# Kernel optimization log

Hardware: AMD Instinct MI355X
Metric: run time of the kernel (lower is better)

## Reference

```python
import jax, jax.numpy as jnp
import numpy as np

B, S, E, H = 4, 2048, 1024, 16
D = E // H

def setup_inputs() -> dict:
    key = jax.random.key(0)
    ks = jax.random.split(key, 8)
    sc = lambda fan_in: 1.0 / np.sqrt(fan_in)
    return {
        "query": jax.random.normal(ks[0], (B, S, E), jnp.float32),
        "Wq": jax.random.normal(ks[1], (E, E), jnp.float32) * sc(E),
        "bq": jnp.zeros((E,), jnp.float32),
        "Wk": jax.random.normal(ks[2], (E, E), jnp.float32) * sc(E),
        "bk": jnp.zeros((E,), jnp.float32),
        "Wv": jax.random.normal(ks[3], (E, E), jnp.float32) * sc(E),
        "bv": jnp.zeros((E,), jnp.float32),
        "Wo": jax.random.normal(ks[4], (E, E), jnp.float32) * sc(E),
        "bo": jnp.zeros((E,), jnp.float32),
        "Wm1": jax.random.normal(ks[5], (E // 4, E), jnp.float32) * sc(E),
        "bm1": jnp.zeros((E // 4,), jnp.float32),
        "Wm2": jax.random.normal(ks[6], (E, E // 4), jnp.float32) * sc(E // 4),
        "bm2": jnp.zeros((E,), jnp.float32),
        "dopamine": jnp.ones((1,), jnp.float32),
        "serotonin": jnp.ones((1,), jnp.float32),
        "norepinephrine": jnp.ones((1,), jnp.float32),
        "acetylcholine": jnp.ones((1,), jnp.float32),
        "attn_scale": jnp.ones((1,), jnp.float32),
        "attn_bias": jnp.zeros((1,), jnp.float32),
    }

def reference(query, Wq, bq, Wk, bk, Wv, bv, Wo, bo,
              Wm1, bm1, Wm2, bm2,
              dopamine, serotonin, norepinephrine, acetylcholine,
              attn_scale, attn_bias):
    scale = D ** (-0.5)
    # projections (nn.Linear: y = x @ W.T + b)
    q = (query @ Wq.T + bq).reshape(B, S, H, D).transpose(0, 2, 1, 3)  # [B,H,S,D]
    k = (query @ Wk.T + bk).reshape(B, S, H, D).transpose(0, 2, 1, 3)
    v = (query @ Wv.T + bv).reshape(B, S, H, D).transpose(0, 2, 1, 3)
    scores = jnp.einsum('bhqd,bhkd->bhqk', q, k) * scale  # [B,H,S,S]
    probs = jax.nn.softmax(scores, axis=-1)
    attn = jnp.einsum('bhqk,bhkd->bhqd', probs, v)  # [B,H,S,D]
    # neuromodulation: MLP on query, summed scalar-weighted effects / 4
    mod = jax.nn.relu(query @ Wm1.T + bm1) @ Wm2.T + bm2  # [B,S,E]
    nm_gain = (dopamine + serotonin + norepinephrine + acetylcholine) / 4.0  # [1]
    neuromod = (mod * nm_gain).reshape(B, S, H, D).transpose(0, 2, 1, 3)  # [B,H,S,D]
    attn = (attn * attn_scale + attn_bias) * (1.0 + neuromod)
    attn = attn.transpose(0, 2, 1, 3).reshape(B, S, E)
    return attn @ Wo.T + bo
```

## Files before the change

### kernel.cpp

```cpp
#include <hip/hip_runtime.h>
#include <hip/hip_bf16.h>
#include <cstdint>

#define PB 4
#define PS 2048
#define PE 1024
#define PH 16
#define PD 64
#define PM (PB * PS)

typedef __attribute__((ext_vector_type(8))) _Float16 half8;
typedef __attribute__((ext_vector_type(4))) float f32x4;

#define MFMAH __builtin_amdgcn_mfma_f32_16x16x32_f16

#define GLOAD_LDS(gp, lp) __builtin_amdgcn_global_load_lds(                    \
    (const __attribute__((address_space(1))) void*)(gp),                       \
    (__attribute__((address_space(3))) void*)(lp), 16, 0, 0)

#if __has_builtin(__builtin_amdgcn_exp2f)
#define FAST_EXP2 1
#define QSC (0.125f * 1.4426950408889634f)
#define FTHR 11.5415603f
#define EXP_P(x) __builtin_amdgcn_exp2f(x)
#else
#define FAST_EXP2 0
#define QSC 0.125f
#define FTHR 8.f
#define EXP_P(x) __expf(x)
#endif

__device__ inline unsigned short h16(float x) {
    _Float16 h = (_Float16)x;
    unsigned short u;
    __builtin_memcpy(&u, &h, 2);
    return u;
}
__device__ inline float f16tof(unsigned short u) {
    _Float16 h;
    __builtin_memcpy(&h, &u, 2);
    return (float)h;
}
__device__ inline unsigned pkrtz(float a, float b) {
    auto p = __builtin_amdgcn_cvt_pkrtz(a, b);
    unsigned u;
    __builtin_memcpy(&u, &p, 4);
    return u;
}

__global__ __launch_bounds__(256)
void split_all(const float* __restrict__ q,   const float* __restrict__ wq,
               const float* __restrict__ wk,  const float* __restrict__ wv,
               const float* __restrict__ wo,  const float* __restrict__ wm1,
               const float* __restrict__ wm2,
               unsigned short* qh,  unsigned short* wqh, unsigned short* wkh,
               unsigned short* wvh, unsigned short* woh,
               unsigned short* m1h, unsigned short* m2h)
{
    const int b = blockIdx.x;
    const float* src; unsigned short* dst; int base;
    if      (b <  8192) { src = q;   dst = qh;  base = 0;     }
    else if (b <  9216) { src = wq;  dst = wqh; base = 8192;  }
    else if (b < 10240) { src = wk;  dst = wkh; base = 9216;  }
    else if (b < 11264) { src = wv;  dst = wvh; base = 10240; }
    else if (b < 12288) { src = wo;  dst = woh; base = 11264; }
    else if (b < 12544) { src = wm1; dst = m1h; base = 12288; }
    else                { src = wm2; dst = m2h; base = 12544; }
    const int i = (b - base) * 256 + threadIdx.x;
    float4 f = ((const float4*)src)[i];
    ushort4 h;
    h.x = h16(f.x); h.y = h16(f.y); h.z = h16(f.z); h.w = h16(f.w);
    ((ushort4*)dst)[i] = h;
}

__global__ __launch_bounds__(512, 2)
void gemm_qkv(const unsigned short* __restrict__ Ah,
              const unsigned short* __restrict__ Wqh,
              const unsigned short* __restrict__ Wkh,
              const unsigned short* __restrict__ Wvh,
              const float* __restrict__ bq, const float* __restrict__ bk,
              const float* __restrict__ bv,
              unsigned short* __restrict__ qh16, unsigned short* __restrict__ kf,
              unsigned short* __restrict__ vtf)
{
    __shared__ int4 ldsq[8192];
    char* const lds = (char*)ldsq;
    const int K = PE;

    const int tid  = threadIdx.x;
    const int lane = tid & 63;
    const int w    = tid >> 6;
    const int lq   = lane & 15;
    const int lg   = lane >> 4;
    const int wr   = w >> 2;
    const int wc   = w & 3;
    const int m0   = blockIdx.x * 128;
    const int n0   = blockIdx.y * 128;

    const int plane = w >> 1;
    const unsigned short* const gp =
        (plane == 0) ? Ah  + (size_t)m0 * K :
        (plane == 1) ? Wqh + (size_t)n0 * K :
        (plane == 2) ? Wkh + (size_t)n0 * K :
                       Wvh + (size_t)n0 * K;
    const int pbase = plane * 16384;
    const int ch0   = (w & 1) * 8;
    const int scol8 = (((lane & 7) ^ (lane >> 3)) << 3);
    const int lrow8 = lane >> 3;

    auto ISSUE = [&](int k0, int bufn) {
        #pragma unroll
        for (int r = 0; r < 8; ++r) {
            const int c   = ch0 + r;
            const int row = c * 8 + lrow8;
            GLOAD_LDS(gp + (size_t)row * K + k0 + scol8,
                      lds + bufn * 65536 + pbase + c * 1024 + 16 * lane);
        }
    };

    f32x4 acc[3][4][2];
    #pragma unroll
    for (int o = 0; o < 3; ++o)
        #pragma unroll
        for (int mt = 0; mt < 4; ++mt)
            #pragma unroll
            for (int nt = 0; nt < 2; ++nt)
                acc[o][mt][nt] = (f32x4){0.f, 0.f, 0.f, 0.f};

    ISSUE(0, 0);
    __syncthreads();

    int buf = 0;
    for (int k0 = 0; k0 < K; k0 += 64) {
        if (k0 + 64 < K) ISSUE(k0 + 64, buf ^ 1);

        const char* const L = lds + buf * 65536;
        #pragma unroll
        for (int kh = 0; kh < 2; ++kh) {
            half8 af[4];
            #pragma unroll
            for (int mt = 0; mt < 4; ++mt) {
                const int row = 64 * wr + 16 * mt + lq;
                const int off = row * 128 + ((kh * 64 + 16 * lg) ^ ((row & 7) << 4));
                af[mt] = *(const half8*)(L + off);
            }
            #pragma unroll
            for (int o = 0; o < 3; ++o) {
                #pragma unroll
                for (int nt = 0; nt < 2; ++nt) {
                    const int row = 32 * wc + 16 * nt + lq;
                    const int off = row * 128 + ((kh * 64 + 16 * lg) ^ ((row & 7) << 4));
                    half8 bf = *(const half8*)(L + 16384 * (o + 1) + off);
                    #pragma unroll
                    for (int mt = 0; mt < 4; ++mt)
                        acc[o][mt][nt] = MFMAH(af[mt], bf, acc[o][mt][nt], 0, 0, 0);
                }
            }
        }
        __syncthreads();
        buf ^= 1;
    }

    #pragma unroll
    for (int nt = 0; nt < 2; ++nt) {
        const int n = n0 + 32 * wc + 16 * nt + lq;
        const int h = n >> 6, d = n & 63;
        const float bqv = bq[n], bkv = bk[n], bvv = bv[n];
        #pragma unroll
        for (int mt = 0; mt < 4; ++mt) {
            #pragma unroll
            for (int j = 0; j < 4; ++j) {
                const int m = m0 + 64 * wr + 16 * mt + 4 * lg + j;
                const int b = m >> 11, s = m & 2047;
                qh16[((size_t)(b * PH + h) * PS + s) * PD + d] =
                    h16((acc[0][mt][nt][j] + bqv) * QSC);
                kf[((size_t)(b * PH + h) * PS + s) * PD + d] =
                    h16(acc[1][mt][nt][j] + bkv);
                const int scol = (s & ~63) + ((mt & 1) << 5) + (lg << 3)
                               + ((mt >> 1) << 2) + j;
                vtf[((size_t)(b * PH + h) * PD + d) * PS + scol] =
                    h16(acc[2][mt][nt][j] + bvv);
            }
        }
    }
}

template<int MODE, bool RELU>
__global__ __launch_bounds__(256, 2)
void gemm_pl(const unsigned short* __restrict__ Ah,
             const unsigned short* __restrict__ Bh,
             const float* __restrict__ bias, float* __restrict__ C,
             unsigned short* __restrict__ Oh,
             int M, int N, int K)
{
    __shared__ int4 ldsq[4096];
    char* const lds = (char*)ldsq;

    const int tid  = threadIdx.x;
    const int lane = tid & 63;
    const int w    = tid >> 6;
    const int lq   = lane & 15;
    const int lg   = lane >> 4;
    const int wm   = (w >> 1) * 64;
    const int wn   = (w & 1) * 64;
    const int m0   = blockIdx.x * 128;
    const int n0   = blockIdx.y * 128;

    const unsigned short* const gp =
        (w < 2) ? Ah + (size_t)m0 * K : Bh + (size_t)n0 * K;
    const int pb    = (w < 2) ? 0 : 16384;
    const int ch0   = (w & 1) * 8;
    const int scol8 = (((lane & 7) ^ (lane >> 3)) << 3);
    const int lrow8 = lane >> 3;

    auto ISSUE = [&](int k0, int bufn) {
        #pragma unroll
        for (int r = 0; r < 8; ++r) {
            const int c   = ch0 + r;
            const int row = c * 8 + lrow8;
            GLOAD_LDS(gp + (size_t)row * K + k0 + scol8,
                      lds + bufn * 32768 + pb + c * 1024 + 16 * lane);
        }
    };

    f32x4 acc[4][4];
    #pragma unroll
    for (int mt = 0; mt < 4; ++mt)
        #pragma unroll
        for (int nt = 0; nt < 4; ++nt)
            acc[mt][nt] = (f32x4){0.f, 0.f, 0.f, 0.f};

    ISSUE(0, 0);
    __syncthreads();

    int buf = 0;
    for (int k0 = 0; k0 < K; k0 += 64) {
        if (k0 + 64 < K) ISSUE(k0 + 64, buf ^ 1);

        const char* const L = lds + buf * 32768;
        #pragma unroll
        for (int kh = 0; kh < 2; ++kh) {
            half8 af[4];
            #pragma unroll
            for (int mt = 0; mt < 4; ++mt) {
                const int row = wm + 16 * mt + lq;
                const int off = row * 128 + ((kh * 64 + 16 * lg) ^ ((row & 7) << 4));
                af[mt] = *(const half8*)(L + off);
            }
            #pragma unroll
            for (int nt = 0; nt < 4; ++nt) {
                const int row = wn + 16 * nt + lq;
                const int off = row * 128 + ((kh * 64 + 16 * lg) ^ ((row & 7) << 4));
                half8 bf = *(const half8*)(L + 16384 + off);
                #pragma unroll
                for (int mt = 0; mt < 4; ++mt)
                    acc[mt][nt] = MFMAH(af[mt], bf, acc[mt][nt], 0, 0, 0);
            }
        }
        __syncthreads();
        buf ^= 1;
    }

    #pragma unroll
    for (int nt = 0; nt < 4; ++nt) {
        const int n  = n0 + wn + 16 * nt + lq;
        const float bv = bias[n];
        #pragma unroll
        for (int mt = 0; mt < 4; ++mt) {
            #pragma unroll
            for (int j = 0; j < 4; ++j) {
                const int m = m0 + wm + 16 * mt + 4 * lg + j;
                float v = acc[mt][nt][j] + bv;
                if (RELU) v = fmaxf(v, 0.f);
                if (MODE == 0) {
                    C[(size_t)m * N + n] = v;
                } else {
                    Oh[(size_t)m * N + n] = h16(v);
                }
            }
        }
    }
}

typedef __attribute__((ext_vector_type(8))) short short8;
#define MFMA16 __builtin_amdgcn_mfma_f32_16x16x32_bf16
__device__ inline unsigned short bf16rn(float x) {
    unsigned u = __builtin_bit_cast(unsigned, x);
    u += 0x7FFFu + ((u >> 16) & 1u);
    return (unsigned short)(u >> 16);
}
__device__ inline float bf16tof(unsigned short h) {
    unsigned u = ((unsigned)h) << 16;
    return __builtin_bit_cast(float, u);
}
__device__ inline void split2(float x, unsigned short& h, unsigned short& l) {
    h = bf16rn(x);
    l = bf16rn(x - bf16tof(h));
}

template<int MODE, bool RELU>
__global__ __launch_bounds__(256, 2)
void gemm_nt(const float* __restrict__ A, const float* __restrict__ Bw,
             const float* __restrict__ bias, float* __restrict__ C,
             unsigned short* __restrict__ Ohi,
             int M, int N, int K,
             const float* __restrict__ attn,
             const float* __restrict__ g0, const float* __restrict__ g1,
             const float* __restrict__ g2, const float* __restrict__ g3,
             const float* __restrict__ asc, const float* __restrict__ abi)
{
    __shared__ int4 ldsq[4096];
    char* const lds = (char*)ldsq;

    const int tid  = threadIdx.x;
    const int lane = tid & 63;
    const int w    = tid >> 6;
    const int lq   = lane & 15;
    const int lg   = lane >> 4;
    const int wm   = (w >> 1) * 64;
    const int wn   = (w & 1) * 64;
    const int m0   = blockIdx.x * 128;
    const int n0   = blockIdx.y * 128;

    const int irow = tid >> 3;
    const int ic8  = (tid & 7) * 8;
    const int woff = (ic8 * 2);

    f32x4 acc[4][4];
    #pragma unroll
    for (int mt = 0; mt < 4; ++mt)
        #pragma unroll
        for (int nt = 0; nt < 4; ++nt)
            acc[mt][nt] = (f32x4){0.f, 0.f, 0.f, 0.f};

    for (int k0 = 0; k0 < K; k0 += 64) {
        #pragma unroll
        for (int mat = 0; mat < 2; ++mat) {
            const float* const src = mat ? Bw : A;
            const int rbase = mat ? n0 : m0;
            const int pbase = mat ? 32768 : 0;
            #pragma unroll
            for (int r = 0; r < 4; ++r) {
                const int row = irow + 32 * r;
                const float* p = src + (size_t)(rbase + row) * K + k0 + ic8;
                float4 f0 = *(const float4*)p;
                float4 f1 = *(const float4*)(p + 4);
                short8 vh, vl;
                {
                    unsigned short h, l;
                    split2(f0.x, h, l); vh[0] = (short)h; vl[0] = (short)l;
                    split2(f0.y, h, l); vh[1] = (short)h; vl[1] = (short)l;
                    split2(f0.z, h, l); vh[2] = (short)h; vl[2] = (short)l;
                    split2(f0.w, h, l); vh[3] = (short)h; vl[3] = (short)l;
                    split2(f1.x, h, l); vh[4] = (short)h; vl[4] = (short)l;
                    split2(f1.y, h, l); vh[5] = (short)h; vl[5] = (short)l;
                    split2(f1.z, h, l); vh[6] = (short)h; vl[6] = (short)l;
                    split2(f1.w, h, l); vh[7] = (short)h; vl[7] = (short)l;
                }
                const int off = row * 128 + (woff ^ ((row & 7) << 4));
                *(short8*)(lds + pbase + off)         = vh;
                *(short8*)(lds + pbase + 16384 + off) = vl;
            }
        }
        __syncthreads();

        #pragma unroll
        for (int kh = 0; kh < 2; ++kh) {
            short8 afh[4], afl[4];
            #pragma unroll
            for (int mt = 0; mt < 4; ++mt) {
                const int row = wm + 16 * mt + lq;
                const int off = row * 128 + ((kh * 64 + 16 * lg) ^ ((row & 7) << 4));
                afh[mt] = *(const short8*)(lds + off);
                afl[mt] = *(const short8*)(lds + 16384 + off);
            }
            #pragma unroll
            for (int nt = 0; nt < 4; ++nt) {
                const int row = wn + 16 * nt + lq;
                const int off = row * 128 + ((kh * 64 + 16 * lg) ^ ((row & 7) << 4));
                short8 bfh = *(const short8*)(lds + 32768 + off);
                short8 bfl = *(const short8*)(lds + 49152 + off);
                #pragma unroll
                for (int mt = 0; mt < 4; ++mt) {
                    acc[mt][nt] = MFMA16(afh[mt], bfh, acc[mt][nt], 0, 0, 0);
                    acc[mt][nt] = MFMA16(afh[mt], bfl, acc[mt][nt], 0, 0, 0);
                    acc[mt][nt] = MFMA16(afl[mt], bfh, acc[mt][nt], 0, 0, 0);
                }
            }
        }
        __syncthreads();
    }

    float gain = 0.f, ascv = 0.f, abiv = 0.f;
    if (MODE == 2) {
        gain = 0.25f * (*g0 + *g1 + *g2 + *g3);
        ascv = *asc;
        abiv = *abi;
    }

    #pragma unroll
    for (int nt = 0; nt < 4; ++nt) {
        const int n  = n0 + wn + 16 * nt + lq;
        const float bv = bias[n];
        #pragma unroll
        for (int mt = 0; mt < 4; ++mt) {
            #pragma unroll
            for (int j = 0; j < 4; ++j) {
                const int m = m0 + wm + 16 * mt + 4 * lg + j;
                float v = acc[mt][nt][j] + bv;
                if (RELU) v = fmaxf(v, 0.f);
                if (MODE == 0) {
                    C[(size_t)m * N + n] = v;
                } else if (MODE == 1) {
                    const int b = m >> 11, s = m & 2047;
                    const int h = n >> 6, d = n & 63;
                    Ohi[((size_t)(b * PH + h) * PS + s) * PD + d] = h16(v * QSC);
                } else if (MODE == 3) {
                    const int b = m >> 11, s = m & 2047;
                    const int h = n >> 6, d = n & 63;
                    Ohi[((size_t)(b * PH + h) * PS + s) * PD + d] = h16(v);
                } else if (MODE == 4) {
                    const int b = m >> 11;
                    const int h = n >> 6, d = n & 63;
                    const int scol = (m & 2047 & ~63) + ((mt & 1) << 5)
                                   + (lg << 3) + ((mt >> 1) << 2) + j;
                    Ohi[((size_t)(b * PH + h) * PD + d) * PS + scol] = h16(v);
                } else {
                    const int b = m >> 11, s = m & 2047;
                    const int h = n >> 6, d = n & 63;
                    const float av = attn[((size_t)(b * PH + h) * PS + s) * PD + d];
                    C[(size_t)m * N + n] = (av * ascv + abiv) * (1.f + v * gain);
                }
            }
        }
    }
}

template<int FUSE>
__global__ __launch_bounds__(256, 4)
void flash_mfma(const unsigned short* __restrict__ qh16,
                const unsigned short* __restrict__ kf,
                const unsigned short* __restrict__ vtf,
                const unsigned short* __restrict__ modh,
                const float* __restrict__ g0, const float* __restrict__ g1,
                const float* __restrict__ g2, const float* __restrict__ g3,
                const float* __restrict__ asc, const float* __restrict__ abi,
                unsigned short* __restrict__ afh, float* __restrict__ attn)
{
    __shared__ int4 ldsv[2048];
    char* const ldsb = (char*)ldsv;

    const int tid  = threadIdx.x;
    const int lane = tid & 63;
    const int w    = tid >> 6;
    const int lq   = lane & 15;
    const int lg   = lane >> 4;

    const int L  = blockIdx.x + (blockIdx.y << 4) + (blockIdx.z << 8);
    const int nL = ((L & 7) << 7) + (L >> 3);
    const int bh = nL >> 4;
    const int q0 = (nL & 15) * 128 + w * 32;

    const size_t kbase = (size_t)bh * PS * PD;
    const size_t vbase = (size_t)bh * PD * PS;

    const unsigned short* const gp = (w < 2) ? kf + kbase : vtf + vbase;
    const bool isK = (w < 2);
    const int ch0   = (w & 1) * 4;
    const int scol8 = (((lane & 7) ^ (lane >> 3)) << 3);
    const int lrow8 = lane >> 3;

    auto ISSUE = [&](int kt, int bufn) {
        #pragma unroll
        for (int r = 0; r < 4; ++r) {
            const int c   = ch0 + r;
            const int row = c * 8 + lrow8;
            const size_t goff = isK ? (size_t)(kt + row) * PD + scol8
                                    : (size_t)row * PS + kt + scol8;
            GLOAD_LDS(gp + goff,
                      ldsb + bufn * 16384 + (isK ? 0 : 8192) + c * 1024 + 16 * lane);
        }
    };

    const half8 onesh = {(_Float16)1.f, (_Float16)1.f, (_Float16)1.f,
                         (_Float16)1.f, (_Float16)1.f, (_Float16)1.f,
                         (_Float16)1.f, (_Float16)1.f};

    half8 qh[2][2];
    #pragma unroll
    for (int u = 0; u < 2; ++u) {
        const unsigned short* qp =
            qh16 + ((size_t)bh * PS + q0 + 16 * u + lq) * PD + 8 * lg;
        qh[u][0] = *(const half8*)(qp);
        qh[u][1] = *(const half8*)(qp + 32);
    }

    f32x4 ot[2][4];
    #pragma unroll
    for (int u = 0; u < 2; ++u)
        #pragma unroll
        for (int mt = 0; mt < 4; ++mt)
            ot[u][mt] = (f32x4){0.f, 0.f, 0.f, 0.f};
    f32x4 lacc[2] = {{0.f,0.f,0.f,0.f}, {0.f,0.f,0.f,0.f}};
    float m_run[2] = {0.f, 0.f};

    ISSUE(0, 0);
    __syncthreads();

    int buf = 0;
    for (int kti = 0; kti < PS / 64; ++kti) {
        const bool pf = (kti + 1 < PS / 64);
        if (pf) ISSUE((kti + 1) * 64, buf ^ 1);

        const char* const L2 = ldsb + buf * 16384;

        f32x4 st[2][4];
        __builtin_amdgcn_s_setprio(1);
        #pragma unroll
        for (int mt = 0; mt < 4; ++mt) {
            const int row = 16 * mt + lq;
            const int swz = (row & 7) << 4;
            const char* kr = L2 + row * 128;
            half8 a0 = *(const half8*)(kr + ((16 * lg) ^ swz));
            half8 a1 = *(const half8*)(kr + ((64 + 16 * lg) ^ swz));
            #pragma unroll
            for (int u = 0; u < 2; ++u) {
                const float nm = -m_run[u];
                f32x4 acc = {nm, nm, nm, nm};
                acc = MFMAH(a0, qh[u][0], acc, 0, 0, 0);
                acc = MFMAH(a1, qh[u][1], acc, 0, 0, 0);
                st[u][mt] = acc;
            }
        }
        __builtin_amdgcn_s_setprio(0);

        half8 pb[2][2];
        #pragma unroll
        for (int u = 0; u < 2; ++u) {
            float a0 = fmaxf(fmaxf(st[u][0][0], st[u][0][1]), st[u][0][2]);
            float a1 = fmaxf(fmaxf(st[u][0][3], st[u][1][0]), st[u][1][1]);
            float a2 = fmaxf(fmaxf(st[u][1][2], st[u][1][3]), st[u][2][0]);
            float a3 = fmaxf(fmaxf(st[u][2][1], st[u][2][2]), st[u][2][3]);
            float a4 = fmaxf(fmaxf(st[u][3][0], st[u][3][1]), st[u][3][2]);
            float b0 = fmaxf(fmaxf(a0, a1), a2);
            float b1 = fmaxf(fmaxf(a3, a4), st[u][3][3]);
            float lmax = fmaxf(b0, b1);
            if (!__all(lmax <= FTHR)) {
                float pmax = fmaxf(lmax, __shfl_xor(lmax, 16));
                pmax = fmaxf(pmax, __shfl_xor(pmax, 32));
                float corr = EXP_P(-pmax);
                m_run[u] += pmax;
                #pragma unroll
                for (int j = 0; j < 4; ++j)
                    lacc[u][j] *= corr;
                #pragma unroll
                for (int mt = 0; mt < 4; ++mt)
                    #pragma unroll
                    for (int j = 0; j < 4; ++j) {
                        ot[u][mt][j] *= corr;
                        st[u][mt][j] -= pmax;
                    }
            }
            #pragma unroll
            for (int mt = 0; mt < 4; ++mt)
                #pragma unroll
                for (int j = 0; j < 4; ++j)
                    st[u][mt][j] = EXP_P(st[u][mt][j]);
            #pragma unroll
            for (int t = 0; t < 2; ++t) {
                unsigned w0 = pkrtz(st[u][t][0],     st[u][t][1]);
                unsigned w1 = pkrtz(st[u][t][2],     st[u][t][3]);
                unsigned w2 = pkrtz(st[u][t + 2][0], st[u][t + 2][1]);
                unsigned w3 = pkrtz(st[u][t + 2][2], st[u][t + 2][3]);
                uint4 pw = make_uint4(w0, w1, w2, w3);
                __builtin_memcpy(&pb[u][t], &pw, 16);
            }
            lacc[u] = MFMAH(onesh, pb[u][0], lacc[u], 0, 0, 0);
            lacc[u] = MFMAH(onesh, pb[u][1], lacc[u], 0, 0, 0);
        }

        __builtin_amdgcn_s_setprio(1);
        #pragma unroll
        for (int t = 0; t < 2; ++t) {
            #pragma unroll
            for (int mt = 0; mt < 4; ++mt) {
                const int row = 16 * mt + lq;
                const int swz = (row & 7) << 4;
                const char* vr = L2 + 8192 + row * 128;
                half8 vv = *(const half8*)(vr + ((t * 64 + 16 * lg) ^ swz));
                #pragma unroll
                for (int u = 0; u < 2; ++u)
                    ot[u][mt] = MFMAH(vv, pb[u][t], ot[u][mt], 0, 0, 0);
            }
        }
        __builtin_amdgcn_s_setprio(0);

        __syncthreads();
        buf ^= 1;
    }

    if (FUSE) {
        const float gain = 0.25f * (*g0 + *g1 + *g2 + *g3);
        const float ascv = *asc, abiv = *abi;
        const int bb = bh >> 4, hh = bh & 15;
        #pragma unroll
        for (int u = 0; u < 2; ++u) {
            const int m = bb * PS + q0 + 16 * u + lq;
            const unsigned short* mp = modh + (size_t)m * PE + hh * 64 + 4 * lg;
            unsigned short* op = afh + (size_t)m * PE + hh * 64 + 4 * lg;
            const float inv = 1.f / lacc[u][0];
            #pragma unroll
            for (int mt = 0; mt < 4; ++mt) {
                ushort4 mv = *(const ushort4*)(mp + 16 * mt);
                ushort4 ov;
                ov.x = h16((ot[u][mt][0] * inv * ascv + abiv) * (1.f + f16tof(mv.x) * gain));
                ov.y = h16((ot[u][mt][1] * inv * ascv + abiv) * (1.f + f16tof(mv.y) * gain));
                ov.z = h16((ot[u][mt][2] * inv * ascv + abiv) * (1.f + f16tof(mv.z) * gain));
                ov.w = h16((ot[u][mt][3] * inv * ascv + abiv) * (1.f + f16tof(mv.w) * gain));
                *(ushort4*)(op + 16 * mt) = ov;
            }
        }
    } else {
        #pragma unroll
        for (int u = 0; u < 2; ++u) {
            const float inv = 1.f / lacc[u][0];
            float* op = attn + ((size_t)bh * PS + q0 + 16 * u + lq) * PD + 4 * lg;
            #pragma unroll
            for (int mt = 0; mt < 4; ++mt) {
                float4 o;
                o.x = ot[u][mt][0] * inv; o.y = ot[u][mt][1] * inv;
                o.z = ot[u][mt][2] * inv; o.w = ot[u][mt][3] * inv;
                *(float4*)(op + 16 * mt) = o;
            }
        }
    }
}

extern "C" void kernel_launch(void* const* d_in, const int* in_sizes, int n_in,
                              void* d_out, int out_size, void* d_ws, size_t ws_size,
                              hipStream_t stream)
{
    const float* query = (const float*)d_in[0];
    const float* Wq  = (const float*)d_in[1];  const float* bq  = (const float*)d_in[2];
    const float* Wk  = (const float*)d_in[3];  const float* bk  = (const float*)d_in[4];
    const float* Wv  = (const float*)d_in[5];  const float* bv  = (const float*)d_in[6];
    const float* Wo  = (const float*)d_in[7];  const float* bo  = (const float*)d_in[8];
    const float* Wm1 = (const float*)d_in[9];  const float* bm1 = (const float*)d_in[10];
    const float* Wm2 = (const float*)d_in[11]; const float* bm2 = (const float*)d_in[12];
    const float* dop = (const float*)d_in[13];
    const float* ser = (const float*)d_in[14];
    const float* nor = (const float*)d_in[15];
    const float* ach = (const float*)d_in[16];
    const float* asc = (const float*)d_in[17];
    const float* abi = (const float*)d_in[18];
    float* out = (float*)d_out;

    char* wsb = (char*)d_ws;
    float*          attnb = (float*)wsb;
    unsigned short* kf    = (unsigned short*)(wsb + (32u << 20));
    unsigned short* vtf   = (unsigned short*)(wsb + (48u << 20));

    dim3 blk(256);
    const bool presplit = (ws_size >= 161480704ull);

    if (presplit) {
        unsigned short* h1h   = (unsigned short*)(wsb + (64u << 20));
        unsigned short* afh   = (unsigned short*)(wsb + (72u << 20));
        unsigned short* qh16  = (unsigned short*)(wsb + (88u << 20));
        unsigned short* qh    = (unsigned short*)(wsb + (104u << 20));
        unsigned short* modh  = (unsigned short*)(wsb + (120u << 20));
        unsigned short* wqh   = (unsigned short*)(wsb + (136u << 20));
        unsigned short* wkh   = (unsigned short*)(wsb + (138u << 20));
        unsigned short* wvh   = (unsigned short*)(wsb + (140u << 20));
        unsigned short* woh   = (unsigned short*)(wsb + (142u << 20));
        unsigned short* m1h   = (unsigned short*)(wsb + (144u << 20));
        unsigned short* m2h   = (unsigned short*)(wsb + (145u << 20));

        split_all<<<12800, blk, 0, stream>>>(
            query, Wq, Wk, Wv, Wo, Wm1, Wm2,
            qh, wqh, wkh, wvh, woh, m1h, m2h);

        gemm_qkv<<<dim3(PM / 128, PE / 128), dim3(512), 0, stream>>>(
            qh, wqh, wkh, wvh, bq, bk, bv, qh16, kf, vtf);

        gemm_pl<5, true><<<dim3(PM / 128, 256 / 128), blk, 0, stream>>>(
            qh, m1h, bm1, nullptr, h1h, PM, 256, PE);
        gemm_pl<5, false><<<dim3(PM / 128, PE / 128), blk, 0, stream>>>(
            h1h, m2h, bm2, nullptr, modh, PM, PE, 256);

        flash_mfma<1><<<dim3(PS / 128, PH, PB), blk, 0, stream>>>(
            qh16, kf, vtf, modh, dop, ser, nor, ach, asc, abi,
            afh, nullptr);

        gemm_pl<0, false><<<dim3(PM / 128, PE / 128), blk, 0, stream>>>(
            afh, woh, bo, out, nullptr, PM, PE, PE);
    } else {
        float* h1    = (float*)(wsb + (64u << 20));
        float* attnf = (float*)(wsb + (72u << 20));
        unsigned short* qh16 = (unsigned short*)(wsb + (72u << 20));

        gemm_nt<1, false><<<dim3(PM / 128, PE / 128), blk, 0, stream>>>(
            query, Wq, bq, nullptr, qh16, PM, PE, PE,
            nullptr, nullptr, nullptr, nullptr, nullptr, nullptr, nullptr);
        gemm_nt<3, false><<<dim3(PM / 128, PE / 128), blk, 0, stream>>>(
            query, Wk, bk, nullptr, kf, PM, PE, PE,
            nullptr, nullptr, nullptr, nullptr, nullptr, nullptr, nullptr);
        gemm_nt<4, false><<<dim3(PM / 128, PE / 128), blk, 0, stream>>>(
            query, Wv, bv, nullptr, vtf, PM, PE, PE,
            nullptr, nullptr, nullptr, nullptr, nullptr, nullptr, nullptr);
        gemm_nt<0, true><<<dim3(PM / 128, 256 / 128), blk, 0, stream>>>(
            query, Wm1, bm1, h1, nullptr, PM, 256, PE,
            nullptr, nullptr, nullptr, nullptr, nullptr, nullptr, nullptr);

        flash_mfma<0><<<dim3(PS / 128, PH, PB), blk, 0, stream>>>(
            qh16, kf, vtf, nullptr, nullptr, nullptr, nullptr, nullptr,
            nullptr, nullptr, nullptr, attnb);

        gemm_nt<2, false><<<dim3(PM / 128, PE / 128), blk, 0, stream>>>(
            h1, Wm2, bm2, attnf, nullptr, PM, PE, 256,
            attnb, dop, ser, nor, ach, asc, abi);
        gemm_nt<0, false><<<dim3(PM / 128, PE / 128), blk, 0, stream>>>(
            attnf, Wo, bo, out, nullptr, PM, PE, PE,
            nullptr, nullptr, nullptr, nullptr, nullptr, nullptr, nullptr);
    }
}
```

Baseline: 201.2 us.

## Fuse fp32-to-fp16 query conversion into QKV and MLP1 GEMM loaders

Removes the separate conversion of the query activation to fp16. The QKV GEMM and a new MLP1 GEMM now load fp32 query tiles into registers, convert them to fp16 and store them swizzled into LDS, while the weight tiles still use direct global-to-LDS loads. This drops one full write and read of an fp16 copy of the query. In exchange, each GEMM reads twice the bytes for A (fp32), query is converted twice, the kernels use more registers, and occupancy is lowered to one block per CU in the launch bounds.

```diff
diff --git a/kernel.cpp b/kernel.cpp
--- a/kernel.cpp
+++ b/kernel.cpp
@@ -47,25 +47,27 @@
     __builtin_memcpy(&u, &p, 4);
     return u;
 }
+__device__ inline unsigned pk2rn(float a, float b) {
+    unsigned u = (unsigned)h16(a) | ((unsigned)h16(b) << 16);
+    return u;
+}
 
 __global__ __launch_bounds__(256)
-void split_all(const float* __restrict__ q,   const float* __restrict__ wq,
-               const float* __restrict__ wk,  const float* __restrict__ wv,
-               const float* __restrict__ wo,  const float* __restrict__ wm1,
-               const float* __restrict__ wm2,
-               unsigned short* qh,  unsigned short* wqh, unsigned short* wkh,
-               unsigned short* wvh, unsigned short* woh,
-               unsigned short* m1h, unsigned short* m2h)
+void split_w(const float* __restrict__ wq,  const float* __restrict__ wk,
+             const float* __restrict__ wv,  const float* __restrict__ wo,
+             const float* __restrict__ wm1, const float* __restrict__ wm2,
+             unsigned short* wqh, unsigned short* wkh,
+             unsigned short* wvh, unsigned short* woh,
+             unsigned short* m1h, unsigned short* m2h)
 {
     const int b = blockIdx.x;
     const float* src; unsigned short* dst; int base;
-    if      (b <  8192) { src = q;   dst = qh;  base = 0;     }
-    else if (b <  9216) { src = wq;  dst = wqh; base = 8192;  }
-    else if (b < 10240) { src = wk;  dst = wkh; base = 9216;  }
-    else if (b < 11264) { src = wv;  dst = wvh; base = 10240; }
-    else if (b < 12288) { src = wo;  dst = woh; base = 11264; }
-    else if (b < 12544) { src = wm1; dst = m1h; base = 12288; }
-    else                { src = wm2; dst = m2h; base = 12544; }
+    if      (b < 1024) { src = wq;  dst = wqh; base = 0;    }
+    else if (b < 2048) { src = wk;  dst = wkh; base = 1024; }
+    else if (b < 3072) { src = wv;  dst = wvh; base = 2048; }
+    else if (b < 4096) { src = wo;  dst = woh; base = 3072; }
+    else if (b < 4352) { src = wm1; dst = m1h; base = 4096; }
+    else               { src = wm2; dst = m2h; base = 4352; }
     const int i = (b - base) * 256 + threadIdx.x;
     float4 f = ((const float4*)src)[i];
     ushort4 h;
@@ -73,8 +75,8 @@
     ((ushort4*)dst)[i] = h;
 }
 
-__global__ __launch_bounds__(512, 2)
-void gemm_qkv(const unsigned short* __restrict__ Ah,
+__global__ __launch_bounds__(512, 1)
+void gemm_qkv(const float* __restrict__ Aq,
               const unsigned short* __restrict__ Wqh,
               const unsigned short* __restrict__ Wkh,
               const unsigned short* __restrict__ Wvh,
@@ -97,24 +99,37 @@
     const int m0   = blockIdx.x * 128;
     const int n0   = blockIdx.y * 128;
 
-    const int plane = w >> 1;
-    const unsigned short* const gp =
-        (plane == 0) ? Ah  + (size_t)m0 * K :
-        (plane == 1) ? Wqh + (size_t)n0 * K :
-        (plane == 2) ? Wkh + (size_t)n0 * K :
-                       Wvh + (size_t)n0 * K;
-    const int pbase = plane * 16384;
-    const int ch0   = (w & 1) * 8;
     const int scol8 = (((lane & 7) ^ (lane >> 3)) << 3);
     const int lrow8 = lane >> 3;
 
-    auto ISSUE = [&](int k0, int bufn) {
-        #pragma unroll
-        for (int r = 0; r < 8; ++r) {
-            const int c   = ch0 + r;
-            const int row = c * 8 + lrow8;
-            GLOAD_LDS(gp + (size_t)row * K + k0 + scol8,
-                      lds + bufn * 65536 + pbase + c * 1024 + 16 * lane);
+    const int arow = tid >> 2;
+    const int agc0 = (2 * tid) & 7;
+    const int aswz = (arow & 7) << 4;
+    const float* const asrc0 = Aq + (size_t)(m0 + arow) * K + agc0 * 8;
+    const int ad0 = arow * 128 + ((agc0 * 16) ^ aswz);
+    const int ad1 = arow * 128 + (((agc0 + 1) * 16) ^ aswz);
+
+    auto LOADA = [&](int k0, float4* a) {
+        const float4* p = (const float4*)(asrc0 + k0);
+        a[0] = p[0]; a[1] = p[1]; a[2] = p[2]; a[3] = p[3];
+    };
+    auto CVTW = [&](const float4* a, int bufn) {
+        uint4 g0 = make_uint4(pk2rn(a[0].x, a[0].y), pk2rn(a[0].z, a[0].w),
+                              pk2rn(a[1].x, a[1].y), pk2rn(a[1].z, a[1].w));
+        uint4 g1 = make_uint4(pk2rn(a[2].x, a[2].y), pk2rn(a[2].z, a[2].w),
+                              pk2rn(a[3].x, a[3].y), pk2rn(a[3].z, a[3].w));
+        *(uint4*)(lds + bufn * 65536 + ad0) = g0;
+        *(uint4*)(lds + bufn * 65536 + ad1) = g1;
+    };
+    auto WISSUE = [&](int k0, int bufn) {
+        #pragma unroll
+        for (int r = 0; r < 6; ++r) {
+            const int c = w * 6 + r;
+            const int p = c >> 4;
+            const int lc = c & 15;
+            const unsigned short* wp = (p == 0) ? Wqh : (p == 1) ? Wkh : Wvh;
+            GLOAD_LDS(wp + (size_t)(n0 + lc * 8 + lrow8) * K + k0 + scol8,
+                      lds + bufn * 65536 + (p + 1) * 16384 + lc * 1024 + 16 * lane);
         }
     };
 
@@ -127,12 +142,22 @@
             for (int nt = 0; nt < 2; ++nt)
                 acc[o][mt][nt] = (f32x4){0.f, 0.f, 0.f, 0.f};
 
-    ISSUE(0, 0);
+    {
+        float4 a0[4];
+        LOADA(0, a0);
+        WISSUE(0, 0);
+        CVTW(a0, 0);
+    }
     __syncthreads();
 
     int buf = 0;
     for (int k0 = 0; k0 < K; k0 += 64) {
-        if (k0 + 64 < K) ISSUE(k0 + 64, buf ^ 1);
+        const bool more = (k0 + 64 < K);
+        float4 an[4];
+        if (more) {
+            LOADA(k0 + 64, an);
+            WISSUE(k0 + 64, buf ^ 1);
+        }
 
         const char* const L = lds + buf * 65536;
         #pragma unroll
@@ -157,6 +182,7 @@
                 }
             }
         }
+        if (more) CVTW(an, buf ^ 1);
         __syncthreads();
         buf ^= 1;
     }
@@ -180,6 +206,124 @@
                                + ((mt >> 1) << 2) + j;
                 vtf[((size_t)(b * PH + h) * PD + d) * PS + scol] =
                     h16(acc[2][mt][nt][j] + bvv);
+            }
+        }
+    }
+}
+
+__global__ __launch_bounds__(256, 1)
+void gemm_m1(const float* __restrict__ Aq,
+             const unsigned short* __restrict__ Bh,
+             const float* __restrict__ bias,
+             unsigned short* __restrict__ Oh)
+{
+    __shared__ int4 ldsq[4096];
+    char* const lds = (char*)ldsq;
+    const int K = PE, N = 256;
+
+    const int tid  = threadIdx.x;
+    const int lane = tid & 63;
+    const int w    = tid >> 6;
+    const int lq   = lane & 15;
+    const int lg   = lane >> 4;
+    const int wm   = (w >> 1) * 64;
+    const int wn   = (w & 1) * 64;
+    const int m0   = blockIdx.x * 128;
+    const int n0   = blockIdx.y * 128;
+
+    const int scol8 = (((lane & 7) ^ (lane >> 3)) << 3);
+    const int lrow8 = lane >> 3;
+
+    const int arow = tid >> 1;
+    const int agc0 = (tid & 1) * 4;
+    const int aswz = (arow & 7) << 4;
+    const float* const asrc0 = Aq + (size_t)(m0 + arow) * K + agc0 * 8;
+
+    auto LOADA = [&](int k0, float4* a) {
+        const float4* p = (const float4*)(asrc0 + k0);
+        #pragma unroll
+        for (int i = 0; i < 8; ++i) a[i] = p[i];
+    };
+    auto CVTW = [&](const float4* a, int bufn) {
+        #pragma unroll
+        for (int g = 0; g < 4; ++g) {
+            uint4 gv = make_uint4(pk2rn(a[2*g].x, a[2*g].y),
+                                  pk2rn(a[2*g].z, a[2*g].w),
+                                  pk2rn(a[2*g+1].x, a[2*g+1].y),
+                                  pk2rn(a[2*g+1].z, a[2*g+1].w));
+            const int off = arow * 128 + (((agc0 + g) * 16) ^ aswz);
+            *(uint4*)(lds + bufn * 32768 + off) = gv;
+        }
+    };
+    auto WISSUE = [&](int k0, int bufn) {
+        #pragma unroll
+        for (int r = 0; r < 4; ++r) {
+            const int c = w * 4 + r;
+            GLOAD_LDS(Bh + (size_t)(n0 + c * 8 + lrow8) * K + k0 + scol8,
+                      lds + bufn * 32768 + 16384 + c * 1024 + 16 * lane);
+        }
+    };
+
+    f32x4 acc[4][4];
+    #pragma unroll
+    for (int mt = 0; mt < 4; ++mt)
+        #pragma unroll
+        for (int nt = 0; nt < 4; ++nt)
+            acc[mt][nt] = (f32x4){0.f, 0.f, 0.f, 0.f};
+
+    {
+        float4 a0[8];
+        LOADA(0, a0);
+        WISSUE(0, 0);
+        CVTW(a0, 0);
+    }
+    __syncthreads();
+
+    int buf = 0;
+    for (int k0 = 0; k0 < K; k0 += 64) {
+        const bool more = (k0 + 64 < K);
+        float4 an[8];
+        if (more) {
+            LOADA(k0 + 64, an);
+            WISSUE(k0 + 64, buf ^ 1);
+        }
+
+        const char* const L = lds + buf * 32768;
+        #pragma unroll
+        for (int kh = 0; kh < 2; ++kh) {
+            half8 af[4];
+            #pragma unroll
+            for (int mt = 0; mt < 4; ++mt) {
+                const int row = wm + 16 * mt + lq;
+                const int off = row * 128 + ((kh * 64 + 16 * lg) ^ ((row & 7) << 4));
+                af[mt] = *(const half8*)(L + off);
+            }
+            #pragma unroll
+            for (int nt = 0; nt < 4; ++nt) {
+                const int row = wn + 16 * nt + lq;
+                const int off = row * 128 + ((kh * 64 + 16 * lg) ^ ((row & 7) << 4));
+                half8 bf = *(const half8*)(L + 16384 + off);
+                #pragma unroll
+                for (int mt = 0; mt < 4; ++mt)
+                    acc[mt][nt] = MFMAH(af[mt], bf, acc[mt][nt], 0, 0, 0);
+            }
+        }
+        if (more) CVTW(an, buf ^ 1);
+        __syncthreads();
+        buf ^= 1;
+    }
+
+    #pragma unroll
+    for (int nt = 0; nt < 4; ++nt) {
+        const int n  = n0 + wn + 16 * nt + lq;
+        const float bv = bias[n];
+        #pragma unroll
+        for (int mt = 0; mt < 4; ++mt) {
+            #pragma unroll
+            for (int j = 0; j < 4; ++j) {
+                const int m = m0 + wm + 16 * mt + 4 * lg + j;
+                float v = fmaxf(acc[mt][nt][j] + bv, 0.f);
+                Oh[(size_t)m * N + n] = h16(v);
             }
         }
     }
@@ -667,7 +811,6 @@
         unsigned short* h1h   = (unsigned short*)(wsb + (64u << 20));
         unsigned short* afh   = (unsigned short*)(wsb + (72u << 20));
         unsigned short* qh16  = (unsigned short*)(wsb + (88u << 20));
-        unsigned short* qh    = (unsigned short*)(wsb + (104u << 20));
         unsigned short* modh  = (unsigned short*)(wsb + (120u << 20));
         unsigned short* wqh   = (unsigned short*)(wsb + (136u << 20));
         unsigned short* wkh   = (unsigned short*)(wsb + (138u << 20));
@@ -676,15 +819,15 @@
         unsigned short* m1h   = (unsigned short*)(wsb + (144u << 20));
         unsigned short* m2h   = (unsigned short*)(wsb + (145u << 20));
 
-        split_all<<<12800, blk, 0, stream>>>(
-            query, Wq, Wk, Wv, Wo, Wm1, Wm2,
-            qh, wqh, wkh, wvh, woh, m1h, m2h);
+        split_w<<<4608, blk, 0, stream>>>(
+            Wq, Wk, Wv, Wo, Wm1, Wm2,
+            wqh, wkh, wvh, woh, m1h, m2h);
 
         gemm_qkv<<<dim3(PM / 128, PE / 128), dim3(512), 0, stream>>>(
-            qh, wqh, wkh, wvh, bq, bk, bv, qh16, kf, vtf);
-
-        gemm_pl<5, true><<<dim3(PM / 128, 256 / 128), blk, 0, stream>>>(
-            qh, m1h, bm1, nullptr, h1h, PM, 256, PE);
+            query, wqh, wkh, wvh, bq, bk, bv, qh16, kf, vtf);
+
+        gemm_m1<<<dim3(PM / 128, 256 / 128), blk, 0, stream>>>(
+            query, m1h, bm1, h1h);
         gemm_pl<5, false><<<dim3(PM / 128, PE / 128), blk, 0, stream>>>(
             h1h, m2h, bm2, nullptr, modh, PM, PE, 256);
 
```

After: 324.4 us. 1.61x slower.

## Halve QKV GEMM N-tile to 64 for smaller LDS and higher occupancy

Applied to the files above, without the earlier changes.

The fused QKV projection kernel now uses a 128x64 output tile per block instead of 128x128, which halves the per-wave accumulators and cuts the double-buffered LDS footprint from 128KB to 80KB. The load plan is reworked so each wave issues five 8-row chunks across the A tile and the three weight tiles, and launch bounds ask for four blocks per CU. The aim is more resident blocks to hide latency and a grid with twice as many blocks. In exchange the A tile is re-read from global memory twice as often and each wave does fewer MFMAs per LDS read, lowering arithmetic intensity.

```diff
diff --git a/kernel.cpp b/kernel.cpp
--- a/kernel.cpp
+++ b/kernel.cpp
@@ -73,7 +73,7 @@
     ((ushort4*)dst)[i] = h;
 }
 
-__global__ __launch_bounds__(512, 2)
+__global__ __launch_bounds__(512, 4)
 void gemm_qkv(const unsigned short* __restrict__ Ah,
               const unsigned short* __restrict__ Wqh,
               const unsigned short* __restrict__ Wkh,
@@ -83,7 +83,7 @@
               unsigned short* __restrict__ qh16, unsigned short* __restrict__ kf,
               unsigned short* __restrict__ vtf)
 {
-    __shared__ int4 ldsq[8192];
+    __shared__ int4 ldsq[5120];
     char* const lds = (char*)ldsq;
     const int K = PE;
 
@@ -95,37 +95,38 @@
     const int wr   = w >> 2;
     const int wc   = w & 3;
     const int m0   = blockIdx.x * 128;
-    const int n0   = blockIdx.y * 128;
-
-    const int plane = w >> 1;
-    const unsigned short* const gp =
-        (plane == 0) ? Ah  + (size_t)m0 * K :
-        (plane == 1) ? Wqh + (size_t)n0 * K :
-        (plane == 2) ? Wkh + (size_t)n0 * K :
-                       Wvh + (size_t)n0 * K;
-    const int pbase = plane * 16384;
-    const int ch0   = (w & 1) * 8;
+    const int n0   = blockIdx.y * 64;
+
     const int scol8 = (((lane & 7) ^ (lane >> 3)) << 3);
     const int lrow8 = lane >> 3;
 
     auto ISSUE = [&](int k0, int bufn) {
         #pragma unroll
-        for (int r = 0; r < 8; ++r) {
-            const int c   = ch0 + r;
-            const int row = c * 8 + lrow8;
-            GLOAD_LDS(gp + (size_t)row * K + k0 + scol8,
-                      lds + bufn * 65536 + pbase + c * 1024 + 16 * lane);
+        for (int r = 0; r < 5; ++r) {
+            const int c = w * 5 + r;
+            const unsigned short* src;
+            int loff;
+            if (c < 16) {
+                src  = Ah + (size_t)(m0 + c * 8 + lrow8) * K;
+                loff = c * 1024;
+            } else {
+                const int o  = (c - 16) >> 3;
+                const int lc = (c - 16) & 7;
+                const unsigned short* wp = (o == 0) ? Wqh : (o == 1) ? Wkh : Wvh;
+                src  = wp + (size_t)(n0 + lc * 8 + lrow8) * K;
+                loff = 16384 + o * 8192 + lc * 1024;
+            }
+            GLOAD_LDS(src + k0 + scol8,
+                      lds + bufn * 40960 + loff + 16 * lane);
         }
     };
 
-    f32x4 acc[3][4][2];
+    f32x4 acc[3][4];
     #pragma unroll
     for (int o = 0; o < 3; ++o)
         #pragma unroll
         for (int mt = 0; mt < 4; ++mt)
-            #pragma unroll
-            for (int nt = 0; nt < 2; ++nt)
-                acc[o][mt][nt] = (f32x4){0.f, 0.f, 0.f, 0.f};
+            acc[o][mt] = (f32x4){0.f, 0.f, 0.f, 0.f};
 
     ISSUE(0, 0);
     __syncthreads();
@@ -134,7 +135,9 @@
     for (int k0 = 0; k0 < K; k0 += 64) {
         if (k0 + 64 < K) ISSUE(k0 + 64, buf ^ 1);
 
-        const char* const L = lds + buf * 65536;
+        const char* const L = lds + buf * 40960;
+        const int brow = 16 * wc + lq;
+        const int bswz = (brow & 7) << 4;
         #pragma unroll
         for (int kh = 0; kh < 2; ++kh) {
             half8 af[4];
@@ -144,43 +147,36 @@
                 const int off = row * 128 + ((kh * 64 + 16 * lg) ^ ((row & 7) << 4));
                 af[mt] = *(const half8*)(L + off);
             }
+            const int boff = brow * 128 + ((kh * 64 + 16 * lg) ^ bswz);
             #pragma unroll
             for (int o = 0; o < 3; ++o) {
+                half8 bf = *(const half8*)(L + 16384 + o * 8192 + boff);
                 #pragma unroll
-                for (int nt = 0; nt < 2; ++nt) {
-                    const int row = 32 * wc + 16 * nt + lq;
-                    const int off = row * 128 + ((kh * 64 + 16 * lg) ^ ((row & 7) << 4));
-                    half8 bf = *(const half8*)(L + 16384 * (o + 1) + off);
-                    #pragma unroll
-                    for (int mt = 0; mt < 4; ++mt)
-                        acc[o][mt][nt] = MFMAH(af[mt], bf, acc[o][mt][nt], 0, 0, 0);
-                }
+                for (int mt = 0; mt < 4; ++mt)
+                    acc[o][mt] = MFMAH(af[mt], bf, acc[o][mt], 0, 0, 0);
             }
         }
         __syncthreads();
         buf ^= 1;
     }
 
+    const int n = n0 + 16 * wc + lq;
+    const int h = n >> 6, d = n & 63;
+    const float bqv = bq[n], bkv = bk[n], bvv = bv[n];
     #pragma unroll
-    for (int nt = 0; nt < 2; ++nt) {
-        const int n = n0 + 32 * wc + 16 * nt + lq;
-        const int h = n >> 6, d = n & 63;
-        const float bqv = bq[n], bkv = bk[n], bvv = bv[n];
-        #pragma unroll
-        for (int mt = 0; mt < 4; ++mt) {
-            #pragma unroll
-            for (int j = 0; j < 4; ++j) {
-                const int m = m0 + 64 * wr + 16 * mt + 4 * lg + j;
-                const int b = m >> 11, s = m & 2047;
-                qh16[((size_t)(b * PH + h) * PS + s) * PD + d] =
-                    h16((acc[0][mt][nt][j] + bqv) * QSC);
-                kf[((size_t)(b * PH + h) * PS + s) * PD + d] =
-                    h16(acc[1][mt][nt][j] + bkv);
-                const int scol = (s & ~63) + ((mt & 1) << 5) + (lg << 3)
-                               + ((mt >> 1) << 2) + j;
-                vtf[((size_t)(b * PH + h) * PD + d) * PS + scol] =
-                    h16(acc[2][mt][nt][j] + bvv);
-            }
+    for (int mt = 0; mt < 4; ++mt) {
+        #pragma unroll
+        for (int j = 0; j < 4; ++j) {
+            const int m = m0 + 64 * wr + 16 * mt + 4 * lg + j;
+            const int b = m >> 11, s = m & 2047;
+            qh16[((size_t)(b * PH + h) * PS + s) * PD + d] =
+                h16((acc[0][mt][j] + bqv) * QSC);
+            kf[((size_t)(b * PH + h) * PS + s) * PD + d] =
+                h16(acc[1][mt][j] + bkv);
+            const int scol = (s & ~63) + ((mt & 1) << 5) + (lg << 3)
+                           + ((mt >> 1) << 2) + j;
+            vtf[((size_t)(b * PH + h) * PD + d) * PS + scol] =
+                h16(acc[2][mt][j] + bvv);
         }
     }
 }
@@ -680,7 +676,7 @@
             query, Wq, Wk, Wv, Wo, Wm1, Wm2,
             qh, wqh, wkh, wvh, woh, m1h, m2h);
 
-        gemm_qkv<<<dim3(PM / 128, PE / 128), dim3(512), 0, stream>>>(
+        gemm_qkv<<<dim3(PM / 128, PE / 64), dim3(512), 0, stream>>>(
             qh, wqh, wkh, wvh, bq, bk, bv, qh16, kf, vtf);
 
         gemm_pl<5, true><<<dim3(PM / 128, 256 / 128), blk, 0, stream>>>(
```

Result: slower. 348.8 us (+73.3%).
